# Performance work log

Measured on AMD Instinct MI355X. Metric: run time of the kernel, lower is better.

The kernel has to match this reference:

```python
import jax, jax.numpy as jnp
import numpy as np

H, W = 128, 128  # image_shape


def setup_inputs() -> dict:
    key = jax.random.key(0)
    Y = jax.random.uniform(key, (32, H * W), dtype=jnp.float32)
    return {"Y": Y}


def reference(Y):
    # Binarize and reshape to images: [B, H, W]
    Yb = (Y > 0.5).astype(jnp.float32).reshape(-1, H, W)

    # DP over rows: heights[i, j] = number of consecutive 1s ending at row i in column j
    def step(h, row):
        h = (h + 1.0) * row
        return h, h

    _, heights = jax.lax.scan(step, jnp.zeros((Yb.shape[0], W), Yb.dtype),
                              jnp.swapaxes(Yb, 0, 1))
    heights = jnp.swapaxes(heights, 0, 1)  # [B, H, W]

    # Largest rectangle in histogram, vectorized over all rows.
    # For bar j: left[j] = prev index k with h[k] < h[j] (else -1),
    #            right[j] = next index k with h[k] < h[j] (else W).
    # This matches the monotonic-stack scan (pops while h[stack[-1]] >= h[i]).
    idx = jnp.arange(W)
    kk = idx[:, None]  # candidate index k (axis -2)
    jj = idx[None, :]  # bar index j (axis -1)
    less = heights[..., :, None] < heights[..., None, :]  # [B, H, W, W]; less[k, j] = h[k] < h[j]
    left = jnp.max(jnp.where(less & (kk < jj), kk, -1), axis=-2)   # [B, H, W]
    right = jnp.min(jnp.where(less & (kk > jj), kk, W), axis=-2)   # [B, H, W]

    area = heights * (right - left - 1).astype(heights.dtype)  # [B, H, W]
    maxarea = jnp.max(area, axis=(1, 2))  # [B]; all-zero image -> 0, matching original
    return maxarea.astype(jnp.int32)[:, None]  # [B, 1]
```

## Files before the change

### kernel.cpp

```cpp
#include <hip/hip_runtime.h>

static constexpr int H = 128;
static constexpr int W = 128;
static constexpr int B = 32;

__global__ __launch_bounds__(W) void lr_rows(const float* __restrict__ Y,
                                             int* __restrict__ partials,
                                             int* __restrict__ out,
                                             int use_atomic) {
    const int task = blockIdx.x;
    const int b = task >> 7;
    const int r = task & (H - 1);
    const int j = threadIdx.x;
    const int wid = j >> 6;
    const int lane = j & 63;
    const float* __restrict__ ycol = Y + (size_t)b * H * W + j;

    unsigned int wmask = 0u;
    #pragma unroll
    for (int k = 0; k < 32; ++k) {
        int t = r - k; t = t < 0 ? 0 : t;
        if (ycol[(size_t)t * W] > 0.5f) wmask |= (1u << k);
    }
    if (r < 32) wmask &= (2u << r) - 1u;
    int h;
    if (wmask == 0xFFFFFFFFu) {
        h = 32;
        int t = r - 32;
        while (t >= 0 && ycol[(size_t)t * W] > 0.5f) { ++h; --t; }
    } else {
        h = __builtin_ctz(~wmask);
    }

    __shared__ unsigned long long tbl[H + 1][2];
    __shared__ int hmx[2];
    __shared__ int wmax[2];
    int hm = h;
    #pragma unroll
    for (int off = 32; off > 0; off >>= 1)
        hm = max(hm, __shfl_xor(hm, off, 64));
    if (lane == 0) { hmx[wid] = hm; tbl[0][wid] = 0ULL; }
    __syncthreads();
    const int hmax = max(hmx[0], hmx[1]);

    for (int t = 1; t <= hmax; ++t) {
        const unsigned long long m = __ballot(h < t);
        if (lane == 0) tbl[t][wid] = m;
    }
    __syncthreads();

    const unsigned long long mlo = tbl[h][0];
    const unsigned long long mhi = tbl[h][1];

    int left, right;
    if (j < 64) {
        const unsigned long long below = mlo & ((1ULL << j) - 1ULL);
        const unsigned long long above = mlo & ~((2ULL << j) - 1ULL);
        left  = below ? 63 - __builtin_clzll(below) : -1;
        right = above ? __builtin_ctzll(above)
                      : (mhi ? 64 + __builtin_ctzll(mhi) : W);
    } else {
        const int jj = j - 64;
        const unsigned long long below = mhi & ((1ULL << jj) - 1ULL);
        const unsigned long long above = mhi & ~((2ULL << jj) - 1ULL);
        left  = below ? 127 - __builtin_clzll(below)
                      : (mlo ? 63 - __builtin_clzll(mlo) : -1);
        right = above ? 64 + __builtin_ctzll(above) : W;
    }

    int area = h * (right - left - 1);

    #pragma unroll
    for (int off = 32; off > 0; off >>= 1)
        area = max(area, __shfl_xor(area, off, 64));
    if (lane == 0) wmax[wid] = area;
    __syncthreads();
    if (j == 0) {
        const int m = max(wmax[0], wmax[1]);
        if (use_atomic) atomicMax(&out[b], m);
        else partials[task] = m;
    }
}

__global__ __launch_bounds__(H) void lr_reduce(const int* __restrict__ partials,
                                               int* __restrict__ out) {
    const int b = blockIdx.x;
    const int j = threadIdx.x;
    __shared__ int wm[2];
    int v = partials[b * H + j];
    #pragma unroll
    for (int off = 32; off > 0; off >>= 1)
        v = max(v, __shfl_xor(v, off, 64));
    if ((j & 63) == 0) wm[j >> 6] = v;
    __syncthreads();
    if (j == 0) out[b] = max(wm[0], wm[1]);
}

extern "C" void kernel_launch(void* const* d_in, const int* in_sizes, int n_in,
                              void* d_out, int out_size, void* d_ws, size_t ws_size,
                              hipStream_t stream) {
    const float* Y = (const float*)d_in[0];
    int* out = (int*)d_out;

    if (ws_size >= (size_t)(B * H) * sizeof(int)) {
        int* partials = (int*)d_ws;
        lr_rows<<<B * H, W, 0, stream>>>(Y, partials, out, 0);
        lr_reduce<<<B, H, 0, stream>>>(partials, out);
    } else {
        hipMemsetAsync(out, 0, (size_t)out_size * sizeof(int), stream);
        lr_rows<<<B * H, W, 0, stream>>>(Y, nullptr, out, 1);
    }
}
```

Before: 13.31 us.

## Process four rows per block sharing one column bit window

Each block now handles four consecutive rows instead of one. It loads a 35-row window per column once and derives all four heights from the shared bitmask. This cuts redundant global loads and quarters the block count, which also shrinks the partial-max reduction to 32 entries per image. In exchange there are more shared-memory tables and serial ballot loops per block, and fewer blocks to spread across the GPU.

```diff
diff --git a/kernel.cpp b/kernel.cpp
--- a/kernel.cpp
+++ b/kernel.cpp
@@ -3,97 +3,111 @@
 static constexpr int H = 128;
 static constexpr int W = 128;
 static constexpr int B = 32;
+static constexpr int RPB = 4;
+static constexpr int WIN = RPB + 31;
+static constexpr int GPB = H / RPB;
 
 __global__ __launch_bounds__(W) void lr_rows(const float* __restrict__ Y,
                                              int* __restrict__ partials,
                                              int* __restrict__ out,
                                              int use_atomic) {
-    const int task = blockIdx.x;
-    const int b = task >> 7;
-    const int r = task & (H - 1);
+    const int blk = blockIdx.x;
+    const int b = blk >> 5;
+    const int rg = blk & (GPB - 1);
+    const int r_top = rg * RPB + (RPB - 1);
     const int j = threadIdx.x;
     const int wid = j >> 6;
     const int lane = j & 63;
     const float* __restrict__ ycol = Y + (size_t)b * H * W + j;
 
-    unsigned int wmask = 0u;
+    unsigned long long mask = 0ULL;
     #pragma unroll
-    for (int k = 0; k < 32; ++k) {
-        int t = r - k; t = t < 0 ? 0 : t;
-        if (ycol[(size_t)t * W] > 0.5f) wmask |= (1u << k);
+    for (int k = 0; k < WIN; ++k) {
+        int t = r_top - k; t = t < 0 ? 0 : t;
+        if (ycol[(size_t)t * W] > 0.5f) mask |= (1ULL << k);
     }
-    if (r < 32) wmask &= (2u << r) - 1u;
-    int h;
-    if (wmask == 0xFFFFFFFFu) {
-        h = 32;
-        int t = r - 32;
-        while (t >= 0 && ycol[(size_t)t * W] > 0.5f) { ++h; --t; }
-    } else {
-        h = __builtin_ctz(~wmask);
+    if (r_top < WIN - 1) mask &= (2ULL << r_top) - 1ULL;
+
+    int h[RPB];
+    #pragma unroll
+    for (int s = 0; s < RPB; ++s) {
+        const int row = r_top - s;
+        int hs = __builtin_ctzll(~(mask >> s));
+        if (hs == WIN - s && row - hs >= 0) {
+            int t = row - hs;
+            while (t >= 0 && ycol[(size_t)t * W] > 0.5f) { ++hs; --t; }
+        }
+        h[s] = hs;
     }
 
-    __shared__ unsigned long long tbl[H + 1][2];
-    __shared__ int hmx[2];
+    __shared__ unsigned long long tbl[RPB][H + 1][2];
+    __shared__ int hmx[RPB][2];
     __shared__ int wmax[2];
-    int hm = h;
+
     #pragma unroll
-    for (int off = 32; off > 0; off >>= 1)
-        hm = max(hm, __shfl_xor(hm, off, 64));
-    if (lane == 0) { hmx[wid] = hm; tbl[0][wid] = 0ULL; }
-    __syncthreads();
-    const int hmax = max(hmx[0], hmx[1]);
-
-    for (int t = 1; t <= hmax; ++t) {
-        const unsigned long long m = __ballot(h < t);
-        if (lane == 0) tbl[t][wid] = m;
+    for (int s = 0; s < RPB; ++s) {
+        int hm = h[s];
+        #pragma unroll
+        for (int off = 32; off > 0; off >>= 1)
+            hm = max(hm, __shfl_xor(hm, off, 64));
+        if (lane == 0) hmx[s][wid] = hm;
     }
     __syncthreads();
 
-    const unsigned long long mlo = tbl[h][0];
-    const unsigned long long mhi = tbl[h][1];
+    #pragma unroll
+    for (int s = 0; s < RPB; ++s) {
+        const int hmax = max(hmx[s][0], hmx[s][1]);
+        for (int t = 1; t <= hmax; ++t) {
+            const unsigned long long m = __ballot(h[s] < t);
+            if (lane == 0) tbl[s][t][wid] = m;
+        }
+    }
+    __syncthreads();
 
-    int left, right;
-    if (j < 64) {
-        const unsigned long long below = mlo & ((1ULL << j) - 1ULL);
-        const unsigned long long above = mlo & ~((2ULL << j) - 1ULL);
-        left  = below ? 63 - __builtin_clzll(below) : -1;
-        right = above ? __builtin_ctzll(above)
-                      : (mhi ? 64 + __builtin_ctzll(mhi) : W);
-    } else {
-        const int jj = j - 64;
-        const unsigned long long below = mhi & ((1ULL << jj) - 1ULL);
-        const unsigned long long above = mhi & ~((2ULL << jj) - 1ULL);
-        left  = below ? 127 - __builtin_clzll(below)
-                      : (mlo ? 63 - __builtin_clzll(mlo) : -1);
-        right = above ? 64 + __builtin_ctzll(above) : W;
+    int acc = 0;
+    #pragma unroll
+    for (int s = 0; s < RPB; ++s) {
+        const unsigned long long mlo = tbl[s][h[s]][0];
+        const unsigned long long mhi = tbl[s][h[s]][1];
+        int left, right;
+        if (j < 64) {
+            const unsigned long long below = mlo & ((1ULL << j) - 1ULL);
+            const unsigned long long above = mlo & ~((2ULL << j) - 1ULL);
+            left  = below ? 63 - __builtin_clzll(below) : -1;
+            right = above ? __builtin_ctzll(above)
+                          : (mhi ? 64 + __builtin_ctzll(mhi) : W);
+        } else {
+            const int jj = j - 64;
+            const unsigned long long below = mhi & ((1ULL << jj) - 1ULL);
+            const unsigned long long above = mhi & ~((2ULL << jj) - 1ULL);
+            left  = below ? 127 - __builtin_clzll(below)
+                          : (mlo ? 63 - __builtin_clzll(mlo) : -1);
+            right = above ? 64 + __builtin_ctzll(above) : W;
+        }
+        acc = max(acc, h[s] * (right - left - 1));
     }
-
-    int area = h * (right - left - 1);
 
     #pragma unroll
     for (int off = 32; off > 0; off >>= 1)
-        area = max(area, __shfl_xor(area, off, 64));
-    if (lane == 0) wmax[wid] = area;
+        acc = max(acc, __shfl_xor(acc, off, 64));
+    if (lane == 0) wmax[wid] = acc;
     __syncthreads();
     if (j == 0) {
         const int m = max(wmax[0], wmax[1]);
         if (use_atomic) atomicMax(&out[b], m);
-        else partials[task] = m;
+        else partials[blk] = m;
     }
 }
 
-__global__ __launch_bounds__(H) void lr_reduce(const int* __restrict__ partials,
-                                               int* __restrict__ out) {
+__global__ __launch_bounds__(64) void lr_reduce(const int* __restrict__ partials,
+                                                int* __restrict__ out) {
     const int b = blockIdx.x;
     const int j = threadIdx.x;
-    __shared__ int wm[2];
-    int v = partials[b * H + j];
+    int v = (j < GPB) ? partials[b * GPB + j] : 0;
     #pragma unroll
     for (int off = 32; off > 0; off >>= 1)
         v = max(v, __shfl_xor(v, off, 64));
-    if ((j & 63) == 0) wm[j >> 6] = v;
-    __syncthreads();
-    if (j == 0) out[b] = max(wm[0], wm[1]);
+    if (j == 0) out[b] = v;
 }
 
 extern "C" void kernel_launch(void* const* d_in, const int* in_sizes, int n_in,
@@ -102,12 +116,12 @@
     const float* Y = (const float*)d_in[0];
     int* out = (int*)d_out;
 
-    if (ws_size >= (size_t)(B * H) * sizeof(int)) {
+    if (ws_size >= (size_t)(B * GPB) * sizeof(int)) {
         int* partials = (int*)d_ws;
-        lr_rows<<<B * H, W, 0, stream>>>(Y, partials, out, 0);
-        lr_reduce<<<B, H, 0, stream>>>(partials, out);
+        lr_rows<<<B * GPB, W, 0, stream>>>(Y, partials, out, 0);
+        lr_reduce<<<B, 64, 0, stream>>>(partials, out);
     } else {
         hipMemsetAsync(out, 0, (size_t)out_size * sizeof(int), stream);
-        lr_rows<<<B * H, W, 0, stream>>>(Y, nullptr, out, 1);
+        lr_rows<<<B * GPB, W, 0, stream>>>(Y, nullptr, out, 1);
     }
 }
```

Result: slower. 14.22 us (+6.9%).
